# Performance work log

Hardware: AMD Instinct MI355X
Metric: run time of the kernel (lower is better)

## Reference

```python
import jax, jax.numpy as jnp
import numpy as np

N = 50000      # nodes
E = 800000     # edges (avg degree 16)
IN = 128       # in_channels = len(cfg.objects)
OC = 16        # out_channels
DIMS = [IN, 16 * OC, 8 * OC, 4 * OC, 2 * OC, OC]  # 128,256,128,64,32,16


def _glorot(key, fan_in, fan_out):
    s = jnp.sqrt(2.0 / (fan_in + fan_out)).astype(jnp.float32)
    return jax.random.normal(key, (fan_in, fan_out), jnp.float32) * s


def setup_inputs() -> dict:
    key = jax.random.key(0)
    ks = jax.random.split(key, 16)
    x = jax.random.normal(ks[0], (N, IN), jnp.float32)
    edge_index = jax.random.randint(ks[1], (2, E), 0, N, dtype=jnp.int32)
    inp = {"x": x, "edge_index": edge_index}
    # four hidden GCN layers
    names = ["1", "2", "3", "4"]
    for i, nm in enumerate(names):
        inp["W" + nm] = _glorot(ks[2 + i], DIMS[i], DIMS[i + 1])
        inp["b" + nm] = jnp.zeros((DIMS[i + 1],), jnp.float32)
    # mu / logstd heads
    inp["Wmu"] = _glorot(ks[10], DIMS[4], DIMS[5])
    inp["bmu"] = jnp.zeros((DIMS[5],), jnp.float32)
    inp["Wls"] = _glorot(ks[11], DIMS[4], DIMS[5])
    inp["bls"] = jnp.zeros((DIMS[5],), jnp.float32)
    return inp


def _gcn_norm(edge_index, n):
    # GCNConv default: add self-loops, symmetric normalization
    sl = jnp.arange(n, dtype=edge_index.dtype)
    row = jnp.concatenate([edge_index[0], sl])  # source
    col = jnp.concatenate([edge_index[1], sl])  # target
    deg = jax.ops.segment_sum(jnp.ones_like(row, jnp.float32), col, num_segments=n)
    dinv = jnp.where(deg > 0, jax.lax.rsqrt(deg), 0.0)
    norm = dinv[row] * dinv[col]  # [E + N]
    return row, col, norm


def _gcn_conv(x, W, b, row, col, norm, n):
    h = x @ W                                   # dense transform [N, F_out]
    msg = h[row] * norm[:, None]                # gather + edge scale
    return jax.ops.segment_sum(msg, col, num_segments=n) + b  # scatter-add


def reference(x, edge_index, W1, b1, W2, b2, W3, b3, W4, b4, Wmu, bmu, Wls, bls):
    n = x.shape[0]
    row, col, norm = _gcn_norm(edge_index, n)
    h = jax.nn.relu(_gcn_conv(x, W1, b1, row, col, norm, n))
    h = jax.nn.relu(_gcn_conv(h, W2, b2, row, col, norm, n))
    h = jax.nn.relu(_gcn_conv(h, W3, b3, row, col, norm, n))
    h = jax.nn.relu(_gcn_conv(h, W4, b4, row, col, norm, n))
    mu = _gcn_conv(h, Wmu, bmu, row, col, norm, n)
    logstd = _gcn_conv(h, Wls, bls, row, col, norm, n)
    return mu, logstd
```

## Files before the change

### kernel.cpp

```cpp
#include <hip/hip_runtime.h>
#include <hip/hip_bf16.h>
#include <stdint.h>

__device__ inline int imin(int a, int b) { return a < b ? a : b; }
__device__ inline int imax(int a, int b) { return a > b ? a : b; }
__device__ inline float bf2f(unsigned short u) {
    return __uint_as_float(((unsigned int)u) << 16);
}
__device__ inline unsigned short f2bf(float v) {
    unsigned int u = __float_as_uint(v);
    unsigned int r = u + 0x7FFFu + ((u >> 16) & 1u);
    return (unsigned short)(r >> 16);
}

typedef __attribute__((ext_vector_type(8))) short short8;
typedef __attribute__((ext_vector_type(4))) float floatx4;


__global__ void k_prologue(int* __restrict__ cnt, int n,
                           const float* __restrict__ x, unsigned short* __restrict__ xb, size_t nx,
                           const float* __restrict__ W1, unsigned short* __restrict__ W1T,
                           const float* __restrict__ W2, unsigned short* __restrict__ W2T,
                           const float* __restrict__ W3, unsigned short* __restrict__ W3T) {
    size_t i = (size_t)blockIdx.x * 256 + threadIdx.x;
    if (i < (size_t)n) { cnt[i] = 0; }
    size_t j = i - n;
    if (i >= (size_t)n && j < nx) { xb[j] = f2bf(x[j]); }
    size_t k = j - nx;
    const int n1 = 128 * 256, n2 = 256 * 128, n3 = 128 * 64;
    if (j >= nx && k < (size_t)(n1 + n2 + n3)) {
        int idx = (int)k;
        if (idx < n1) {
            int kk = idx >> 8, nn = idx & 255;
            W1T[nn * 128 + kk] = f2bf(W1[idx]);
        } else if (idx < n1 + n2) {
            int jj = idx - n1;
            int kk = jj >> 7, nn = jj & 127;
            W2T[nn * 256 + kk] = f2bf(W2[jj]);
        } else {
            int jj = idx - n1 - n2;
            int kk = jj >> 6, nn = jj & 63;
            W3T[nn * 128 + kk] = f2bf(W3[jj]);
        }
    }
}


__global__ void k_count(const int* __restrict__ col, int* __restrict__ cnt,
                        int* __restrict__ rank, int E, int n) {
    int e = blockIdx.x * blockDim.x + threadIdx.x;
    if (e < E) {
        int c = imax(0, imin(col[e], n - 1));
        rank[e] = atomicAdd(&cnt[c], 1);
    }
}

__global__ __launch_bounds__(256) void k_scan1(const int* __restrict__ cnt,
                                               int* __restrict__ partial,
                                               int* __restrict__ bsum, int n) {
    __shared__ int tmp[256];
    int i = blockIdx.x * 256 + threadIdx.x;
    int v = (i < n) ? ((cnt[i] + 3) & ~3) : 0;
    tmp[threadIdx.x] = v;
    __syncthreads();
    #pragma unroll
    for (int s = 1; s < 256; s <<= 1) {
        int t = (threadIdx.x >= s) ? tmp[threadIdx.x - s] : 0;
        __syncthreads();
        tmp[threadIdx.x] += t;
        __syncthreads();
    }
    if (i < n) partial[i] = tmp[threadIdx.x] - v;
    if (threadIdx.x == 255) bsum[blockIdx.x] = tmp[255];
}

__global__ __launch_bounds__(256) void k_scan2(const int* __restrict__ bsum,
                                               int* __restrict__ bsumoff, int nb) {
    __shared__ int tmp[256];
    __shared__ int carry;
    if (threadIdx.x == 0) carry = 0;
    __syncthreads();
    for (int base = 0; base < nb; base += 256) {
        int i = base + threadIdx.x;
        int v = (i < nb) ? bsum[i] : 0;
        tmp[threadIdx.x] = v;
        __syncthreads();
        #pragma unroll
        for (int s = 1; s < 256; s <<= 1) {
            int t = (threadIdx.x >= s) ? tmp[threadIdx.x - s] : 0;
            __syncthreads();
            tmp[threadIdx.x] += t;
            __syncthreads();
        }
        if (i < nb) bsumoff[i] = carry + tmp[threadIdx.x] - v;
        __syncthreads();
        if (threadIdx.x == 0) carry += tmp[255];
        __syncthreads();
    }
}

template <bool USEW>
__global__ __launch_bounds__(256) void k_scan3(const int* __restrict__ partial,
                                               const int* __restrict__ bsumoff,
                                               const int* __restrict__ cnt,
                                               int* __restrict__ offs,
                                               float* __restrict__ dinv,
                                               unsigned long long* __restrict__ edges,
                                               int* __restrict__ csr_src,
                                               int n) {
    int i = blockIdx.x * 256 + threadIdx.x;
    if (i >= n) return;
    int v = partial[i] + bsumoff[blockIdx.x];
    int c = imax(cnt[i], 0);
    offs[i] = v;
    if (i == n - 1) offs[n] = v + ((c + 3) & ~3);
    float d = (float)c + 1.0f;
    dinv[i] = rsqrtf(d);
    int end = v + ((c + 3) & ~3);
    for (int p = v + c; p < end; p++) {
        if (USEW) edges[p] = 0ull;
        else csr_src[p] = 0;
    }
}

template <bool USEW>
__global__ void k_fill(const int* __restrict__ row, const int* __restrict__ col,
                       const int* __restrict__ offs, const int* __restrict__ rank,
                       const float* __restrict__ dinv,
                       unsigned long long* __restrict__ edges, int* __restrict__ csr_src,
                       int E, int n, int cap) {
    int e = blockIdx.x * blockDim.x + threadIdx.x;
    if (e >= E) return;
    int c = imax(0, imin(col[e], n - 1));
    int r = imax(0, imin(row[e], n - 1));
    int pos = offs[c] + rank[e];
    pos = imax(0, imin(pos, cap - 1));
    if (USEW) {
        unsigned long long rec = (unsigned long long)(unsigned)r
                               | ((unsigned long long)__float_as_uint(dinv[r]) << 32);
        edges[pos] = rec;
    } else {
        csr_src[pos] = r;
    }
}


template <int NT, int FOUT, bool EPI>
__global__ __launch_bounds__(256) void k_gemm_mfma(const unsigned short* __restrict__ act,
                                                   const unsigned short* __restrict__ WT,
                                                   unsigned short* __restrict__ H,
                                                   const float* __restrict__ bias,
                                                   int nrows, int Fin) {
    constexpr int CT = NT / 16;
    __shared__ __align__(16) unsigned short sA[128 * 40];
    __shared__ __align__(16) unsigned short sB[NT * 40];
    const int tid = threadIdx.x;
    const int w = tid >> 6;
    const int lane = tid & 63;
    const int quad = lane >> 4;
    const int l15 = lane & 15;
    const int row0 = blockIdx.x * 128;
    const int col0 = blockIdx.y * NT;

    floatx4 acc[2][CT] = {};

    const int sr = tid >> 1;
    const int sp = (tid & 1) * 16;

    for (int k0 = 0; k0 < Fin; k0 += 32) {
        __syncthreads();
        {
            int grow = row0 + sr;
            uint4 v0 = make_uint4(0, 0, 0, 0), v1 = make_uint4(0, 0, 0, 0);
            if (grow < nrows) {
                const uint4* ap = (const uint4*)&act[(size_t)grow * Fin + k0 + sp];
                v0 = ap[0]; v1 = ap[1];
            }
            uint4* dst = (uint4*)&sA[sr * 40 + sp];
            dst[0] = v0; dst[1] = v1;
        }
        if (NT == 128 || tid < 128) {
            const uint4* wp = (const uint4*)&WT[(size_t)(col0 + sr) * Fin + k0 + sp];
            uint4* dst = (uint4*)&sB[sr * 40 + sp];
            dst[0] = wp[0]; dst[1] = wp[1];
        }
        __syncthreads();

        short8 bfr[CT];
        #pragma unroll
        for (int ct = 0; ct < CT; ct++)
            bfr[ct] = *(const short8*)&sB[(ct * 16 + l15) * 40 + quad * 8];
        #pragma unroll
        for (int rt = 0; rt < 2; rt++) {
            short8 afr = *(const short8*)&sA[(w * 32 + rt * 16 + l15) * 40 + quad * 8];
            #pragma unroll
            for (int ct = 0; ct < CT; ct++)
                acc[rt][ct] = __builtin_amdgcn_mfma_f32_16x16x32_bf16(afr, bfr[ct], acc[rt][ct], 0, 0, 0);
        }
    }

    #pragma unroll
    for (int rt = 0; rt < 2; rt++) {
        #pragma unroll
        for (int ct = 0; ct < CT; ct++) {
            int gcol = col0 + ct * 16 + l15;
            #pragma unroll
            for (int r = 0; r < 4; r++) {
                int grow = row0 + w * 32 + rt * 16 + quad * 4 + r;
                if (grow < nrows) {
                    float v = acc[rt][ct][r];
                    if (EPI) v = fmaxf(v + bias[gcol], 0.f);
                    H[(size_t)grow * FOUT + gcol] = f2bf(v);
                }
            }
        }
    }
}


__global__ __launch_bounds__(256) void k_gemm32(const unsigned short* __restrict__ act,
                                                const float* __restrict__ W,
                                                unsigned short* __restrict__ H,
                                                int nrows) {
    __shared__ __align__(16) float sA[32 * 68];
    __shared__ __align__(16) float sW[16 * 32];
    const int tid = threadIdx.x;
    const int row0 = blockIdx.x * 32;
    const int Fin = 64, strA = 68;

    for (int i = tid; i < 32 * Fin; i += 256) {
        int r = i >> 6;
        int k = i & 63;
        float v = 0.f;
        if (row0 + r < nrows) v = bf2f(act[(size_t)row0 * Fin + i]);
        sA[r * strA + k] = v;
    }

    const int rl = tid >> 3;
    const int cg = tid & 7;
    float a0 = 0.f, a1 = 0.f, a2 = 0.f, a3 = 0.f;

    for (int k0 = 0; k0 < Fin; k0 += 16) {
        __syncthreads();
        const float* wsrc = W + (size_t)k0 * 32;
        for (int i = tid; i < 16 * 32; i += 256) sW[i] = wsrc[i];
        __syncthreads();
        #pragma unroll 4
        for (int kk = 0; kk < 16; kk++) {
            float a = sA[rl * strA + k0 + kk];
            float4 wv = *(const float4*)&sW[kk * 32 + cg * 4];
            a0 = fmaf(a, wv.x, a0);
            a1 = fmaf(a, wv.y, a1);
            a2 = fmaf(a, wv.z, a2);
            a3 = fmaf(a, wv.w, a3);
        }
    }

    const int rowi = row0 + rl;
    if (rowi < nrows) {
        unsigned short* hp = &H[(size_t)rowi * 32 + cg * 4];
        hp[0] = f2bf(a0); hp[1] = f2bf(a1); hp[2] = f2bf(a2); hp[3] = f2bf(a3);
    }
}

__global__ void k_gemm_heads(const unsigned short* __restrict__ act,
                             const float* __restrict__ Wmu, const float* __restrict__ Wls,
                             unsigned short* __restrict__ H, int nrows) {
    int idx = blockIdx.x * blockDim.x + threadIdx.x;
    if (idx >= nrows * 32) return;
    int r = idx >> 5;
    int c = idx & 31;
    const float* Wp = (c < 16) ? Wmu : Wls;
    int cc = c & 15;
    float acc = 0.f;
    #pragma unroll 8
    for (int k = 0; k < 32; k++)
        acc = fmaf(bf2f(act[(size_t)r * 32 + k]), Wp[k * 16 + cc], acc);
    H[idx] = f2bf(acc);
}


template <int F, bool RELU, bool HASBIAS, bool USEW>
__global__ __launch_bounds__(256) void k_aggb(const unsigned short* __restrict__ Hb,
                                              unsigned short* __restrict__ out,
                                              const int* __restrict__ offs,
                                              const unsigned long long* __restrict__ edges,
                                              const int* __restrict__ src,
                                              const float* __restrict__ dinv,
                                              const float* __restrict__ bias,
                                              int nnodes, int Ecap) {
    constexpr int TPN = F / 4;
    int t = blockIdx.x * 256 + threadIdx.x;
    int node = t / TPN;
    int ln = t % TPN;
    if (node >= nnodes) return;
    int f0 = 4 * ln;

    float di = dinv[node];
    ushort4 sv = *(const ushort4*)&Hb[(size_t)node * F + f0];
    float acc0 = di * bf2f(sv.x);
    float acc1 = di * bf2f(sv.y);
    float acc2 = di * bf2f(sv.z);
    float acc3 = di * bf2f(sv.w);

    int s0 = offs[node];
    int s1 = offs[node + 1];
    s0 = imax(0, imin(s0, Ecap));
    s1 = imax(s0, imin(s1, Ecap));
    int e = s0;
    for (; e + 16 <= s1; e += 16) {
        int sr[16];
        float wv[16];
        if (USEW) {
            #pragma unroll
            for (int q = 0; q < 8; q++) {
                uint4 pr = *(const uint4*)(edges + e + 2 * q);
                sr[2 * q] = (int)pr.x;     wv[2 * q] = __uint_as_float(pr.y);
                sr[2 * q + 1] = (int)pr.z; wv[2 * q + 1] = __uint_as_float(pr.w);
            }
        } else {
            #pragma unroll
            for (int q = 0; q < 4; q++) {
                int4 a = *(const int4*)(src + e + 4 * q);
                sr[4 * q] = a.x; sr[4 * q + 1] = a.y; sr[4 * q + 2] = a.z; sr[4 * q + 3] = a.w;
            }
            #pragma unroll
            for (int q = 0; q < 16; q++) wv[q] = dinv[sr[q]];
        }
        ushort4 h[16];
        #pragma unroll
        for (int q = 0; q < 16; q++)
            h[q] = *(const ushort4*)&Hb[(size_t)sr[q] * F + f0];
        #pragma unroll
        for (int q = 0; q < 16; q++) {
            acc0 = fmaf(wv[q], bf2f(h[q].x), acc0);
            acc1 = fmaf(wv[q], bf2f(h[q].y), acc1);
            acc2 = fmaf(wv[q], bf2f(h[q].z), acc2);
            acc3 = fmaf(wv[q], bf2f(h[q].w), acc3);
        }
    }
    for (; e < s1; e += 4) {
        int sr[4];
        float wv[4];
        if (USEW) {
            uint4 p0 = *(const uint4*)(edges + e);
            uint4 p1 = *(const uint4*)(edges + e + 2);
            sr[0] = (int)p0.x; wv[0] = __uint_as_float(p0.y);
            sr[1] = (int)p0.z; wv[1] = __uint_as_float(p0.w);
            sr[2] = (int)p1.x; wv[2] = __uint_as_float(p1.y);
            sr[3] = (int)p1.z; wv[3] = __uint_as_float(p1.w);
        } else {
            int4 a = *(const int4*)(src + e);
            sr[0] = a.x; sr[1] = a.y; sr[2] = a.z; sr[3] = a.w;
            #pragma unroll
            for (int q = 0; q < 4; q++) wv[q] = dinv[sr[q]];
        }
        ushort4 h[4];
        #pragma unroll
        for (int q = 0; q < 4; q++)
            h[q] = *(const ushort4*)&Hb[(size_t)sr[q] * F + f0];
        #pragma unroll
        for (int q = 0; q < 4; q++) {
            acc0 = fmaf(wv[q], bf2f(h[q].x), acc0);
            acc1 = fmaf(wv[q], bf2f(h[q].y), acc1);
            acc2 = fmaf(wv[q], bf2f(h[q].z), acc2);
            acc3 = fmaf(wv[q], bf2f(h[q].w), acc3);
        }
    }
    float v0 = di * acc0;
    float v1 = di * acc1;
    float v2 = di * acc2;
    float v3 = di * acc3;
    if (HASBIAS) { v0 += bias[f0]; v1 += bias[f0 + 1]; v2 += bias[f0 + 2]; v3 += bias[f0 + 3]; }
    if (RELU) {
        v0 = fmaxf(v0, 0.f); v1 = fmaxf(v1, 0.f);
        v2 = fmaxf(v2, 0.f); v3 = fmaxf(v3, 0.f);
    }
    ushort4 o;
    o.x = f2bf(v0); o.y = f2bf(v1); o.z = f2bf(v2); o.w = f2bf(v3);
    *(ushort4*)&out[(size_t)node * F + f0] = o;
}

template <bool USEW>
__global__ __launch_bounds__(256) void k_agg_heads(const unsigned short* __restrict__ Hb,
                                                   float* __restrict__ out,
                                                   const int* __restrict__ offs,
                                                   const unsigned long long* __restrict__ edges,
                                                   const int* __restrict__ src,
                                                   const float* __restrict__ dinv,
                                                   const float* __restrict__ bmu, const float* __restrict__ bls,
                                                   int nnodes, int Ecap) {
    constexpr int F = 32, TPN = 8;
    int t = blockIdx.x * 256 + threadIdx.x;
    int node = t / TPN;
    int ln = t % TPN;
    if (node >= nnodes) return;
    int f0 = 4 * ln;

    float di = dinv[node];
    ushort4 sv = *(const ushort4*)&Hb[(size_t)node * F + f0];
    float acc0 = di * bf2f(sv.x);
    float acc1 = di * bf2f(sv.y);
    float acc2 = di * bf2f(sv.z);
    float acc3 = di * bf2f(sv.w);

    int s0 = offs[node];
    int s1 = offs[node + 1];
    s0 = imax(0, imin(s0, Ecap));
    s1 = imax(s0, imin(s1, Ecap));
    int e = s0;
    for (; e + 16 <= s1; e += 16) {
        int sr[16];
        float wv[16];
        if (USEW) {
            #pragma unroll
            for (int q = 0; q < 8; q++) {
                uint4 pr = *(const uint4*)(edges + e + 2 * q);
                sr[2 * q] = (int)pr.x;     wv[2 * q] = __uint_as_float(pr.y);
                sr[2 * q + 1] = (int)pr.z; wv[2 * q + 1] = __uint_as_float(pr.w);
            }
        } else {
            #pragma unroll
            for (int q = 0; q < 4; q++) {
                int4 a = *(const int4*)(src + e + 4 * q);
                sr[4 * q] = a.x; sr[4 * q + 1] = a.y; sr[4 * q + 2] = a.z; sr[4 * q + 3] = a.w;
            }
            #pragma unroll
            for (int q = 0; q < 16; q++) wv[q] = dinv[sr[q]];
        }
        ushort4 h[16];
        #pragma unroll
        for (int q = 0; q < 16; q++)
            h[q] = *(const ushort4*)&Hb[(size_t)sr[q] * F + f0];
        #pragma unroll
        for (int q = 0; q < 16; q++) {
            acc0 = fmaf(wv[q], bf2f(h[q].x), acc0);
            acc1 = fmaf(wv[q], bf2f(h[q].y), acc1);
            acc2 = fmaf(wv[q], bf2f(h[q].z), acc2);
            acc3 = fmaf(wv[q], bf2f(h[q].w), acc3);
        }
    }
    for (; e < s1; e += 4) {
        int sr[4];
        float wv[4];
        if (USEW) {
            uint4 p0 = *(const uint4*)(edges + e);
            uint4 p1 = *(const uint4*)(edges + e + 2);
            sr[0] = (int)p0.x; wv[0] = __uint_as_float(p0.y);
            sr[1] = (int)p0.z; wv[1] = __uint_as_float(p0.w);
            sr[2] = (int)p1.x; wv[2] = __uint_as_float(p1.y);
            sr[3] = (int)p1.z; wv[3] = __uint_as_float(p1.w);
        } else {
            int4 a = *(const int4*)(src + e);
            sr[0] = a.x; sr[1] = a.y; sr[2] = a.z; sr[3] = a.w;
            #pragma unroll
            for (int q = 0; q < 4; q++) wv[q] = dinv[sr[q]];
        }
        ushort4 h[4];
        #pragma unroll
        for (int q = 0; q < 4; q++)
            h[q] = *(const ushort4*)&Hb[(size_t)sr[q] * F + f0];
        #pragma unroll
        for (int q = 0; q < 4; q++) {
            acc0 = fmaf(wv[q], bf2f(h[q].x), acc0);
            acc1 = fmaf(wv[q], bf2f(h[q].y), acc1);
            acc2 = fmaf(wv[q], bf2f(h[q].z), acc2);
            acc3 = fmaf(wv[q], bf2f(h[q].w), acc3);
        }
    }
    const float* bp = (f0 < 16) ? bmu : bls;
    int fb = f0 & 15;
    float v0 = fmaf(di, acc0, bp[fb]);
    float v1 = fmaf(di, acc1, bp[fb + 1]);
    float v2 = fmaf(di, acc2, bp[fb + 2]);
    float v3 = fmaf(di, acc3, bp[fb + 3]);
    float* op = (f0 < 16) ? (out + (size_t)node * 16 + fb)
                          : (out + (size_t)nnodes * 16 + (size_t)node * 16 + fb);
    *(float4*)op = make_float4(v0, v1, v2, v3);
}


template <bool USEW>
static void run_pipeline(void* const* d_in, void* d_out, void* d_ws,
                         int N, int E, hipStream_t stream) {
    const float* x  = (const float*)d_in[0];
    const int* ei   = (const int*)d_in[1];
    const float* W1 = (const float*)d_in[2];
    const float* b1 = (const float*)d_in[3];
    const float* W2 = (const float*)d_in[4];
    const float* b2 = (const float*)d_in[5];
    const float* W3 = (const float*)d_in[6];
    const float* b3 = (const float*)d_in[7];
    const float* W4 = (const float*)d_in[8];
    const float* b4 = (const float*)d_in[9];
    const float* Wmu = (const float*)d_in[10];
    const float* bmu = (const float*)d_in[11];
    const float* Wls = (const float*)d_in[12];
    const float* bls = (const float*)d_in[13];
    const int* row = ei;
    const int* col = ei + E;
    const int nb = (N + 255) / 256;
    const int E8 = E + 8 * N;

    auto align16 = [](char* p) {
        return (char*)(((uintptr_t)p + 15) & ~(uintptr_t)15);
    };
    char* p = (char*)d_ws;
    unsigned short* act = (unsigned short*)p;    p += (size_t)N * 256 * 2;
    unsigned short* H = (unsigned short*)p;      p += (size_t)N * 256 * 2;
    unsigned short* xb = H;
    unsigned short* xa = (unsigned short*)p;     p += (size_t)N * 128 * 2;
    float* dinv = (float*)p;                     p += (size_t)N * 4;
    int* cnt = (int*)p;                          p += (size_t)N * 4;
    int* offs = (int*)p;                         p += (size_t)(N + 1) * 4;
    int* partial = (int*)p;                      p += (size_t)N * 4;
    int* bsum = (int*)p;                         p += (size_t)nb * 4;
    int* bsumoff = (int*)p;                      p += (size_t)nb * 4;
    p = align16(p);
    int* rank = (int*)p;                         p += (size_t)E * 4;
    p = align16(p);
    unsigned short* W1T = (unsigned short*)p;    p += 256 * 128 * 2;
    unsigned short* W2T = (unsigned short*)p;    p += 128 * 256 * 2;
    unsigned short* W3T = (unsigned short*)p;    p += 64 * 128 * 2;
    p = align16(p);
    unsigned long long* edges = nullptr;
    int* csr_src = nullptr;
    if (USEW) edges = (unsigned long long*)p;
    else      csr_src = (int*)p;

    {
        size_t total = (size_t)N + (size_t)N * 128 + (128 * 256 + 256 * 128 + 128 * 64);
        k_prologue<<<(unsigned)((total + 255) / 256), 256, 0, stream>>>(
            cnt, N, x, xb, (size_t)N * 128, W1, W1T, W2, W2T, W3, W3T);
    }
    k_count<<<(E + 255) / 256, 256, 0, stream>>>(col, cnt, rank, E, N);
    k_scan1<<<nb, 256, 0, stream>>>(cnt, partial, bsum, N);
    k_scan2<<<1, 256, 0, stream>>>(bsum, bsumoff, nb);
    k_scan3<USEW><<<nb, 256, 0, stream>>>(partial, bsumoff, cnt, offs, dinv, edges, csr_src, N);
    k_fill<USEW><<<(E + 255) / 256, 256, 0, stream>>>(row, col, offs, rank, dinv, edges, csr_src, E, N, E8);

    const int gx = (N + 127) / 128;
    k_aggb<128, false, false, USEW><<<(unsigned)(((size_t)N * 32 + 255) / 256), 256, 0, stream>>>(xb, xa, offs, edges, csr_src, dinv, nullptr, N, E8);
    k_gemm_mfma<128, 256, true><<<dim3(gx, 2), 256, 0, stream>>>(xa, W1T, act, b1, N, 128);
    k_gemm_mfma<128, 128, false><<<dim3(gx, 1), 256, 0, stream>>>(act, W2T, H, nullptr, N, 256);
    k_aggb<128, true, true, USEW><<<(unsigned)(((size_t)N * 32 + 255) / 256), 256, 0, stream>>>(H, act, offs, edges, csr_src, dinv, b2, N, E8);
    k_gemm_mfma<64, 64, false><<<dim3(gx, 1), 256, 0, stream>>>(act, W3T, H, nullptr, N, 128);
    k_aggb<64, true, true, USEW><<<(unsigned)(((size_t)N * 16 + 255) / 256), 256, 0, stream>>>(H, act, offs, edges, csr_src, dinv, b3, N, E8);
    k_gemm32<<<(N + 31) / 32, 256, 0, stream>>>(act, W4, H, N);
    k_aggb<32, true, true, USEW><<<(unsigned)(((size_t)N * 8 + 255) / 256), 256, 0, stream>>>(H, act, offs, edges, csr_src, dinv, b4, N, E8);
    float* outF = (float*)d_out;
    k_gemm_heads<<<(unsigned)(((size_t)N * 32 + 255) / 256), 256, 0, stream>>>(act, Wmu, Wls, H, N);
    k_agg_heads<USEW><<<(unsigned)(((size_t)N * 8 + 255) / 256), 256, 0, stream>>>(H, outF, offs, edges, csr_src, dinv, bmu, bls, N, E8);
}

extern "C" void kernel_launch(void* const* d_in, const int* in_sizes, int n_in,
                              void* d_out, int out_size, void* d_ws, size_t ws_size,
                              hipStream_t stream) {
    const int N = in_sizes[0] / 128;
    const int E = in_sizes[1] / 2;
    const int nb = (N + 255) / 256;
    const size_t E8 = (size_t)E + 8 * (size_t)N;

    size_t fixed = (size_t)N * 256 * 2 * 2 + (size_t)N * 128 * 2
                 + (size_t)N * 4 * 4 + 4 + (size_t)nb * 8 + (size_t)E * 4
                 + (256 * 128 + 128 * 256 + 64 * 128) * 2 + 128;
    size_t need_w = fixed + E8 * 8;
    if (ws_size >= need_w)
        run_pipeline<true>(d_in, d_out, d_ws, N, E, stream);
    else
        run_pipeline<false>(d_in, d_out, d_ws, N, E, stream);
}
```

Baseline: 351.0 us.

## Fuse whole GCN pipeline into one cooperative persistent kernel with grid syncs

Replaces about fifteen separate kernel launches (CSR build, scans, aggregations, GEMMs, heads) with a single cooperative kernel of 512 blocks. The phases run as grid-stride loops separated by grid.sync(). The aim is to remove per-launch overhead and the idle gaps between dependent kernels. In exchange, occupancy is capped at 512 blocks with launch_bounds(256,2), each phase pays a grid-wide barrier, and the GEMM and aggregation work is tiled less flexibly. The old multi-kernel path is kept as a fallback if the cooperative launch fails.

```diff
diff --git a/kernel.cpp b/kernel.cpp
--- a/kernel.cpp
+++ b/kernel.cpp
@@ -1,6 +1,9 @@
 #include <hip/hip_runtime.h>
+#include <hip/hip_cooperative_groups.h>
 #include <hip/hip_bf16.h>
 #include <stdint.h>
+
+namespace cg = cooperative_groups;
 
 __device__ inline int imin(int a, int b) { return a < b ? a : b; }
 __device__ inline int imax(int a, int b) { return a > b ? a : b; }
@@ -17,18 +20,17 @@
 typedef __attribute__((ext_vector_type(4))) float floatx4;
 
 
-__global__ void k_prologue(int* __restrict__ cnt, int n,
-                           const float* __restrict__ x, unsigned short* __restrict__ xb, size_t nx,
-                           const float* __restrict__ W1, unsigned short* __restrict__ W1T,
-                           const float* __restrict__ W2, unsigned short* __restrict__ W2T,
-                           const float* __restrict__ W3, unsigned short* __restrict__ W3T) {
-    size_t i = (size_t)blockIdx.x * 256 + threadIdx.x;
-    if (i < (size_t)n) { cnt[i] = 0; }
+__device__ inline void prologue_elem(size_t i, int n, int* __restrict__ cnt,
+                                     const float* __restrict__ x, unsigned short* __restrict__ xb, size_t nx,
+                                     const float* __restrict__ W1, unsigned short* __restrict__ W1T,
+                                     const float* __restrict__ W2, unsigned short* __restrict__ W2T,
+                                     const float* __restrict__ W3, unsigned short* __restrict__ W3T) {
+    if (i < (size_t)n) { cnt[i] = 0; return; }
     size_t j = i - n;
-    if (i >= (size_t)n && j < nx) { xb[j] = f2bf(x[j]); }
+    if (j < nx) { xb[j] = f2bf(x[j]); return; }
     size_t k = j - nx;
     const int n1 = 128 * 256, n2 = 256 * 128, n3 = 128 * 64;
-    if (j >= nx && k < (size_t)(n1 + n2 + n3)) {
+    if (k < (size_t)(n1 + n2 + n3)) {
         int idx = (int)k;
         if (idx < n1) {
             int kk = idx >> 8, nn = idx & 255;
@@ -45,72 +47,54 @@
     }
 }
 
-
-__global__ void k_count(const int* __restrict__ col, int* __restrict__ cnt,
-                        int* __restrict__ rank, int E, int n) {
-    int e = blockIdx.x * blockDim.x + threadIdx.x;
-    if (e < E) {
-        int c = imax(0, imin(col[e], n - 1));
-        rank[e] = atomicAdd(&cnt[c], 1);
-    }
-}
-
-__global__ __launch_bounds__(256) void k_scan1(const int* __restrict__ cnt,
-                                               int* __restrict__ partial,
-                                               int* __restrict__ bsum, int n) {
-    __shared__ int tmp[256];
-    int i = blockIdx.x * 256 + threadIdx.x;
+__device__ inline void scan1_chunk(int chunk, int tid, int* __restrict__ tmp,
+                                   const int* __restrict__ cnt,
+                                   int* __restrict__ partial, int* __restrict__ bsum, int n) {
+    int i = chunk * 256 + tid;
     int v = (i < n) ? ((cnt[i] + 3) & ~3) : 0;
-    tmp[threadIdx.x] = v;
+    tmp[tid] = v;
     __syncthreads();
     #pragma unroll
     for (int s = 1; s < 256; s <<= 1) {
-        int t = (threadIdx.x >= s) ? tmp[threadIdx.x - s] : 0;
+        int t = (tid >= s) ? tmp[tid - s] : 0;
         __syncthreads();
-        tmp[threadIdx.x] += t;
+        tmp[tid] += t;
         __syncthreads();
     }
-    if (i < n) partial[i] = tmp[threadIdx.x] - v;
-    if (threadIdx.x == 255) bsum[blockIdx.x] = tmp[255];
-}
-
-__global__ __launch_bounds__(256) void k_scan2(const int* __restrict__ bsum,
-                                               int* __restrict__ bsumoff, int nb) {
-    __shared__ int tmp[256];
-    __shared__ int carry;
-    if (threadIdx.x == 0) carry = 0;
+    if (i < n) partial[i] = tmp[tid] - v;
+    if (tid == 255) bsum[chunk] = tmp[255];
+}
+
+__device__ inline void scan2_block(int tid, int* __restrict__ tmp, int* __restrict__ carry,
+                                   const int* __restrict__ bsum, int* __restrict__ bsumoff, int nb) {
+    if (tid == 0) *carry = 0;
     __syncthreads();
     for (int base = 0; base < nb; base += 256) {
-        int i = base + threadIdx.x;
+        int i = base + tid;
         int v = (i < nb) ? bsum[i] : 0;
-        tmp[threadIdx.x] = v;
+        tmp[tid] = v;
         __syncthreads();
         #pragma unroll
         for (int s = 1; s < 256; s <<= 1) {
-            int t = (threadIdx.x >= s) ? tmp[threadIdx.x - s] : 0;
+            int t = (tid >= s) ? tmp[tid - s] : 0;
             __syncthreads();
-            tmp[threadIdx.x] += t;
+            tmp[tid] += t;
             __syncthreads();
         }
-        if (i < nb) bsumoff[i] = carry + tmp[threadIdx.x] - v;
+        if (i < nb) bsumoff[i] = *carry + tmp[tid] - v;
         __syncthreads();
-        if (threadIdx.x == 0) carry += tmp[255];
+        if (tid == 0) *carry += tmp[255];
         __syncthreads();
     }
 }
 
 template <bool USEW>
-__global__ __launch_bounds__(256) void k_scan3(const int* __restrict__ partial,
-                                               const int* __restrict__ bsumoff,
-                                               const int* __restrict__ cnt,
-                                               int* __restrict__ offs,
-                                               float* __restrict__ dinv,
-                                               unsigned long long* __restrict__ edges,
-                                               int* __restrict__ csr_src,
-                                               int n) {
-    int i = blockIdx.x * 256 + threadIdx.x;
-    if (i >= n) return;
-    int v = partial[i] + bsumoff[blockIdx.x];
+__device__ inline void scan3_elem(int i, int boff,
+                                  const int* __restrict__ partial, const int* __restrict__ cnt,
+                                  int* __restrict__ offs, float* __restrict__ dinv,
+                                  unsigned long long* __restrict__ edges, int* __restrict__ csr_src,
+                                  int n) {
+    int v = partial[i] + boff;
     int c = imax(cnt[i], 0);
     offs[i] = v;
     if (i == n - 1) offs[n] = v + ((c + 3) & ~3);
@@ -124,13 +108,11 @@
 }
 
 template <bool USEW>
-__global__ void k_fill(const int* __restrict__ row, const int* __restrict__ col,
-                       const int* __restrict__ offs, const int* __restrict__ rank,
-                       const float* __restrict__ dinv,
-                       unsigned long long* __restrict__ edges, int* __restrict__ csr_src,
-                       int E, int n, int cap) {
-    int e = blockIdx.x * blockDim.x + threadIdx.x;
-    if (e >= E) return;
+__device__ inline void fill_elem(int e, const int* __restrict__ row, const int* __restrict__ col,
+                                 const int* __restrict__ offs, const int* __restrict__ rank,
+                                 const float* __restrict__ dinv,
+                                 unsigned long long* __restrict__ edges, int* __restrict__ csr_src,
+                                 int n, int cap) {
     int c = imax(0, imin(col[e], n - 1));
     int r = imax(0, imin(row[e], n - 1));
     int pos = offs[c] + rank[e];
@@ -146,21 +128,19 @@
 
 
 template <int NT, int FOUT, bool EPI>
-__global__ __launch_bounds__(256) void k_gemm_mfma(const unsigned short* __restrict__ act,
-                                                   const unsigned short* __restrict__ WT,
-                                                   unsigned short* __restrict__ H,
-                                                   const float* __restrict__ bias,
-                                                   int nrows, int Fin) {
+__device__ void gemm_tile(const unsigned short* __restrict__ act,
+                          const unsigned short* __restrict__ WT,
+                          unsigned short* __restrict__ H,
+                          const float* __restrict__ bias,
+                          int nrows, int Fin, int bx, int by, int tid,
+                          unsigned short* __restrict__ sA, unsigned short* __restrict__ sB) {
     constexpr int CT = NT / 16;
-    __shared__ __align__(16) unsigned short sA[128 * 40];
-    __shared__ __align__(16) unsigned short sB[NT * 40];
-    const int tid = threadIdx.x;
     const int w = tid >> 6;
     const int lane = tid & 63;
     const int quad = lane >> 4;
     const int l15 = lane & 15;
-    const int row0 = blockIdx.x * 128;
-    const int col0 = blockIdx.y * NT;
+    const int row0 = bx * 128;
+    const int col0 = by * NT;
 
     floatx4 acc[2][CT] = {};
 
@@ -218,15 +198,15 @@
 }
 
 
-__global__ __launch_bounds__(256) void k_gemm32(const unsigned short* __restrict__ act,
-                                                const float* __restrict__ W,
-                                                unsigned short* __restrict__ H,
-                                                int nrows) {
-    __shared__ __align__(16) float sA[32 * 68];
-    __shared__ __align__(16) float sW[16 * 32];
-    const int tid = threadIdx.x;
-    const int row0 = blockIdx.x * 32;
+__device__ void gemm32_tile(const unsigned short* __restrict__ act,
+                            const float* __restrict__ W,
+                            unsigned short* __restrict__ H,
+                            int nrows, int bx, int tid,
+                            float* __restrict__ sA, float* __restrict__ sW) {
+    const int row0 = bx * 32;
     const int Fin = 64, strA = 68;
+
+    __syncthreads();
 
     for (int i = tid; i < 32 * Fin; i += 256) {
         int r = i >> 6;
@@ -234,10 +214,11 @@
         float v = 0.f;
         if (row0 + r < nrows) v = bf2f(act[(size_t)row0 * Fin + i]);
         sA[r * strA + k] = v;
+        (void)k;
     }
 
     const int rl = tid >> 3;
-    const int cg = tid & 7;
+    const int cg_ = tid & 7;
     float a0 = 0.f, a1 = 0.f, a2 = 0.f, a3 = 0.f;
 
     for (int k0 = 0; k0 < Fin; k0 += 16) {
@@ -248,7 +229,7 @@
         #pragma unroll 4
         for (int kk = 0; kk < 16; kk++) {
             float a = sA[rl * strA + k0 + kk];
-            float4 wv = *(const float4*)&sW[kk * 32 + cg * 4];
+            float4 wv = *(const float4*)&sW[kk * 32 + cg_ * 4];
             a0 = fmaf(a, wv.x, a0);
             a1 = fmaf(a, wv.y, a1);
             a2 = fmaf(a, wv.z, a2);
@@ -258,16 +239,14 @@
 
     const int rowi = row0 + rl;
     if (rowi < nrows) {
-        unsigned short* hp = &H[(size_t)rowi * 32 + cg * 4];
+        unsigned short* hp = &H[(size_t)rowi * 32 + cg_ * 4];
         hp[0] = f2bf(a0); hp[1] = f2bf(a1); hp[2] = f2bf(a2); hp[3] = f2bf(a3);
     }
 }
 
-__global__ void k_gemm_heads(const unsigned short* __restrict__ act,
-                             const float* __restrict__ Wmu, const float* __restrict__ Wls,
-                             unsigned short* __restrict__ H, int nrows) {
-    int idx = blockIdx.x * blockDim.x + threadIdx.x;
-    if (idx >= nrows * 32) return;
+__device__ inline void heads_one(int idx, const unsigned short* __restrict__ act,
+                                 const float* __restrict__ Wmu, const float* __restrict__ Wls,
+                                 unsigned short* __restrict__ H) {
     int r = idx >> 5;
     int c = idx & 31;
     const float* Wp = (c < 16) ? Wmu : Wls;
@@ -281,19 +260,15 @@
 
 
 template <int F, bool RELU, bool HASBIAS, bool USEW>
-__global__ __launch_bounds__(256) void k_aggb(const unsigned short* __restrict__ Hb,
-                                              unsigned short* __restrict__ out,
-                                              const int* __restrict__ offs,
-                                              const unsigned long long* __restrict__ edges,
-                                              const int* __restrict__ src,
-                                              const float* __restrict__ dinv,
-                                              const float* __restrict__ bias,
-                                              int nnodes, int Ecap) {
-    constexpr int TPN = F / 4;
-    int t = blockIdx.x * 256 + threadIdx.x;
-    int node = t / TPN;
-    int ln = t % TPN;
-    if (node >= nnodes) return;
+__device__ inline void agg_one(int node, int ln,
+                               const unsigned short* __restrict__ Hb,
+                               unsigned short* __restrict__ out,
+                               const int* __restrict__ offs,
+                               const unsigned long long* __restrict__ edges,
+                               const int* __restrict__ src,
+                               const float* __restrict__ dinv,
+                               const float* __restrict__ bias,
+                               int Ecap) {
     int f0 = 4 * ln;
 
     float di = dinv[node];
@@ -382,19 +357,16 @@
 }
 
 template <bool USEW>
-__global__ __launch_bounds__(256) void k_agg_heads(const unsigned short* __restrict__ Hb,
-                                                   float* __restrict__ out,
-                                                   const int* __restrict__ offs,
-                                                   const unsigned long long* __restrict__ edges,
-                                                   const int* __restrict__ src,
-                                                   const float* __restrict__ dinv,
-                                                   const float* __restrict__ bmu, const float* __restrict__ bls,
-                                                   int nnodes, int Ecap) {
-    constexpr int F = 32, TPN = 8;
-    int t = blockIdx.x * 256 + threadIdx.x;
-    int node = t / TPN;
-    int ln = t % TPN;
-    if (node >= nnodes) return;
+__device__ inline void agg_heads_one(int node, int ln,
+                                     const unsigned short* __restrict__ Hb,
+                                     float* __restrict__ out,
+                                     const int* __restrict__ offs,
+                                     const unsigned long long* __restrict__ edges,
+                                     const int* __restrict__ src,
+                                     const float* __restrict__ dinv,
+                                     const float* __restrict__ bmu, const float* __restrict__ bls,
+                                     int nnodes, int Ecap) {
+    constexpr int F = 32;
     int f0 = 4 * ln;
 
     float di = dinv[node];
@@ -479,6 +451,267 @@
     *(float4*)op = make_float4(v0, v1, v2, v3);
 }
 
+
+struct MegaP {
+    const float* x;
+    const int* row; const int* col;
+    const float *W1, *b1, *W2, *b2, *W3, *b3, *W4, *b4, *Wmu, *bmu, *Wls, *bls;
+    unsigned short *act, *H, *xb, *xa, *W1T, *W2T, *W3T;
+    float* dinv;
+    int *cnt, *offs, *partial, *bsum, *bsumoff, *rank;
+    unsigned long long* edges;
+    int* csr_src;
+    float* outF;
+    int N, E, nb, E8;
+};
+
+template <int F, bool RELU, bool HASBIAS, bool USEW>
+__device__ inline void agg_phase(long long g0, long long T,
+                                 const unsigned short* Hb, unsigned short* out,
+                                 const float* bias, const MegaP& P) {
+    constexpr int TPN = F / 4;
+    long long total = (long long)P.N * TPN;
+    for (long long t = g0; t < total; t += T) {
+        int node = (int)(t / TPN);
+        int ln = (int)(t % TPN);
+        agg_one<F, RELU, HASBIAS, USEW>(node, ln, Hb, out, P.offs, P.edges, P.csr_src,
+                                        P.dinv, bias, P.E8);
+    }
+}
+
+template <bool USEW>
+__global__ __launch_bounds__(256, 2) void k_mega(MegaP P) {
+    cg::grid_group grid = cg::this_grid();
+    __shared__ __align__(16) unsigned char SMEM[20480];
+    const int tid = threadIdx.x;
+    const int G = gridDim.x;
+    const long long T = (long long)G * 256;
+    const long long g0 = (long long)blockIdx.x * 256 + tid;
+
+    {
+        size_t total = (size_t)P.N + (size_t)P.N * 128 + (128 * 256 + 256 * 128 + 128 * 64);
+        for (size_t i = (size_t)g0; i < total; i += (size_t)T)
+            prologue_elem(i, P.N, P.cnt, P.x, P.xb, (size_t)P.N * 128,
+                          P.W1, P.W1T, P.W2, P.W2T, P.W3, P.W3T);
+    }
+    grid.sync();
+    for (long long e = g0; e < P.E; e += T) {
+        int c = imax(0, imin(P.col[e], P.N - 1));
+        P.rank[e] = atomicAdd(&P.cnt[c], 1);
+    }
+    grid.sync();
+    {
+        int* tmp = (int*)SMEM;
+        for (int chunk = blockIdx.x; chunk < P.nb; chunk += G) {
+            __syncthreads();
+            scan1_chunk(chunk, tid, tmp, P.cnt, P.partial, P.bsum, P.N);
+        }
+    }
+    grid.sync();
+    if (blockIdx.x == 0) {
+        int* tmp = (int*)SMEM;
+        int* carry = (int*)(SMEM + 1024);
+        scan2_block(tid, tmp, carry, P.bsum, P.bsumoff, P.nb);
+    }
+    grid.sync();
+    for (long long i = g0; i < P.N; i += T)
+        scan3_elem<USEW>((int)i, P.bsumoff[i >> 8], P.partial, P.cnt,
+                         P.offs, P.dinv, P.edges, P.csr_src, P.N);
+    grid.sync();
+    for (long long e = g0; e < P.E; e += T)
+        fill_elem<USEW>((int)e, P.row, P.col, P.offs, P.rank, P.dinv,
+                        P.edges, P.csr_src, P.N, P.E8);
+    grid.sync();
+    agg_phase<128, false, false, USEW>(g0, T, P.xb, P.xa, nullptr, P);
+    grid.sync();
+    {
+        unsigned short* sA = (unsigned short*)SMEM;
+        unsigned short* sB = sA + 128 * 40;
+        int gx = (P.N + 127) >> 7;
+        for (int tile = blockIdx.x; tile < gx * 2; tile += G)
+            gemm_tile<128, 256, true>(P.xa, P.W1T, P.act, P.b1, P.N, 128,
+                                      tile % gx, tile / gx, tid, sA, sB);
+    }
+    grid.sync();
+    {
+        unsigned short* sA = (unsigned short*)SMEM;
+        unsigned short* sB = sA + 128 * 40;
+        int gx = (P.N + 127) >> 7;
+        for (int tile = blockIdx.x; tile < gx; tile += G)
+            gemm_tile<128, 128, false>(P.act, P.W2T, P.H, nullptr, P.N, 256,
+                                       tile, 0, tid, sA, sB);
+    }
+    grid.sync();
+    agg_phase<128, true, true, USEW>(g0, T, P.H, P.act, P.b2, P);
+    grid.sync();
+    {
+        unsigned short* sA = (unsigned short*)SMEM;
+        unsigned short* sB = sA + 128 * 40;
+        int gx = (P.N + 127) >> 7;
+        for (int tile = blockIdx.x; tile < gx; tile += G)
+            gemm_tile<64, 64, false>(P.act, P.W3T, P.H, nullptr, P.N, 128,
+                                     tile, 0, tid, sA, sB);
+    }
+    grid.sync();
+    agg_phase<64, true, true, USEW>(g0, T, P.H, P.act, P.b3, P);
+    grid.sync();
+    {
+        float* sA32 = (float*)SMEM;
+        float* sW = (float*)(SMEM + 32 * 68 * 4);
+        int nt = (P.N + 31) >> 5;
+        for (int tile = blockIdx.x; tile < nt; tile += G)
+            gemm32_tile(P.act, P.W4, P.H, P.N, tile, tid, sA32, sW);
+    }
+    grid.sync();
+    agg_phase<32, true, true, USEW>(g0, T, P.H, P.act, P.b4, P);
+    grid.sync();
+    for (long long idx = g0; idx < (long long)P.N * 32; idx += T)
+        heads_one((int)idx, P.act, P.Wmu, P.Wls, P.H);
+    grid.sync();
+    {
+        constexpr int TPN = 8;
+        long long total = (long long)P.N * TPN;
+        for (long long t = g0; t < total; t += T) {
+            int node = (int)(t / TPN);
+            int ln = (int)(t % TPN);
+            agg_heads_one<USEW>(node, ln, P.H, P.outF, P.offs, P.edges, P.csr_src,
+                                P.dinv, P.bmu, P.bls, P.N, P.E8);
+        }
+    }
+}
+
+
+__global__ void k_prologue(int* cnt, int n, const float* x, unsigned short* xb, size_t nx,
+                           const float* W1, unsigned short* W1T,
+                           const float* W2, unsigned short* W2T,
+                           const float* W3, unsigned short* W3T) {
+    size_t i = (size_t)blockIdx.x * 256 + threadIdx.x;
+    size_t total = (size_t)n + nx + (128 * 256 + 256 * 128 + 128 * 64);
+    if (i < total) prologue_elem(i, n, cnt, x, xb, nx, W1, W1T, W2, W2T, W3, W3T);
+}
+
+__global__ void k_count(const int* col, int* cnt, int* rank, int E, int n) {
+    int e = blockIdx.x * blockDim.x + threadIdx.x;
+    if (e < E) {
+        int c = imax(0, imin(col[e], n - 1));
+        rank[e] = atomicAdd(&cnt[c], 1);
+    }
+}
+
+__global__ __launch_bounds__(256) void k_scan1(const int* cnt, int* partial, int* bsum, int n) {
+    __shared__ int tmp[256];
+    scan1_chunk(blockIdx.x, threadIdx.x, tmp, cnt, partial, bsum, n);
+}
+
+__global__ __launch_bounds__(256) void k_scan2(const int* bsum, int* bsumoff, int nb) {
+    __shared__ int tmp[256];
+    __shared__ int carry;
+    scan2_block(threadIdx.x, tmp, &carry, bsum, bsumoff, nb);
+}
+
+template <bool USEW>
+__global__ __launch_bounds__(256) void k_scan3(const int* partial, const int* bsumoff,
+                                               const int* cnt, int* offs, float* dinv,
+                                               unsigned long long* edges, int* csr_src, int n) {
+    int i = blockIdx.x * 256 + threadIdx.x;
+    if (i < n)
+        scan3_elem<USEW>(i, bsumoff[blockIdx.x], partial, cnt, offs, dinv, edges, csr_src, n);
+}
+
+template <bool USEW>
+__global__ void k_fill(const int* row, const int* col, const int* offs, const int* rank,
+                       const float* dinv, unsigned long long* edges, int* csr_src,
+                       int E, int n, int cap) {
+    int e = blockIdx.x * blockDim.x + threadIdx.x;
+    if (e < E) fill_elem<USEW>(e, row, col, offs, rank, dinv, edges, csr_src, n, cap);
+}
+
+template <int NT, int FOUT, bool EPI>
+__global__ __launch_bounds__(256) void k_gemm_mfma(const unsigned short* act,
+                                                   const unsigned short* WT,
+                                                   unsigned short* H, const float* bias,
+                                                   int nrows, int Fin) {
+    __shared__ __align__(16) unsigned short sA[128 * 40];
+    __shared__ __align__(16) unsigned short sB[NT * 40];
+    gemm_tile<NT, FOUT, EPI>(act, WT, H, bias, nrows, Fin, blockIdx.x, blockIdx.y,
+                             threadIdx.x, sA, sB);
+}
+
+__global__ __launch_bounds__(256) void k_gemm32(const unsigned short* act, const float* W,
+                                                unsigned short* H, int nrows) {
+    __shared__ __align__(16) float sA[32 * 68];
+    __shared__ __align__(16) float sW[16 * 32];
+    gemm32_tile(act, W, H, nrows, blockIdx.x, threadIdx.x, sA, sW);
+}
+
+__global__ void k_gemm_heads(const unsigned short* act, const float* Wmu, const float* Wls,
+                             unsigned short* H, int nrows) {
+    int idx = blockIdx.x * blockDim.x + threadIdx.x;
+    if (idx < nrows * 32) heads_one(idx, act, Wmu, Wls, H);
+}
+
+template <int F, bool RELU, bool HASBIAS, bool USEW>
+__global__ __launch_bounds__(256) void k_aggb(const unsigned short* Hb, unsigned short* out,
+                                              const int* offs, const unsigned long long* edges,
+                                              const int* src, const float* dinv,
+                                              const float* bias, int nnodes, int Ecap) {
+    constexpr int TPN = F / 4;
+    int t = blockIdx.x * 256 + threadIdx.x;
+    int node = t / TPN;
+    int ln = t % TPN;
+    if (node < nnodes)
+        agg_one<F, RELU, HASBIAS, USEW>(node, ln, Hb, out, offs, edges, src, dinv, bias, Ecap);
+}
+
+template <bool USEW>
+__global__ __launch_bounds__(256) void k_agg_heads(const unsigned short* Hb, float* out,
+                                                   const int* offs, const unsigned long long* edges,
+                                                   const int* src, const float* dinv,
+                                                   const float* bmu, const float* bls,
+                                                   int nnodes, int Ecap) {
+    constexpr int TPN = 8;
+    int t = blockIdx.x * 256 + threadIdx.x;
+    int node = t / TPN;
+    int ln = t % TPN;
+    if (node < nnodes)
+        agg_heads_one<USEW>(node, ln, Hb, out, offs, edges, src, dinv, bmu, bls, nnodes, Ecap);
+}
+
+
+struct WsLayout {
+    unsigned short *act, *H, *xb, *xa, *W1T, *W2T, *W3T;
+    float* dinv;
+    int *cnt, *offs, *partial, *bsum, *bsumoff, *rank;
+    unsigned long long* edges;
+    int* csr_src;
+};
+
+static WsLayout layout_ws(void* d_ws, int N, int E, bool usew) {
+    auto align16 = [](char* p) { return (char*)(((uintptr_t)p + 15) & ~(uintptr_t)15); };
+    const int nb = (N + 255) / 256;
+    WsLayout L;
+    char* p = (char*)d_ws;
+    L.act = (unsigned short*)p;   p += (size_t)N * 256 * 2;
+    L.H = (unsigned short*)p;     p += (size_t)N * 256 * 2;
+    L.xb = L.H;
+    L.xa = (unsigned short*)p;    p += (size_t)N * 128 * 2;
+    L.dinv = (float*)p;           p += (size_t)N * 4;
+    L.cnt = (int*)p;              p += (size_t)N * 4;
+    L.offs = (int*)p;             p += (size_t)(N + 1) * 4;
+    L.partial = (int*)p;          p += (size_t)N * 4;
+    L.bsum = (int*)p;             p += (size_t)nb * 4;
+    L.bsumoff = (int*)p;          p += (size_t)nb * 4;
+    p = align16(p);
+    L.rank = (int*)p;             p += (size_t)E * 4;
+    p = align16(p);
+    L.W1T = (unsigned short*)p;   p += 256 * 128 * 2;
+    L.W2T = (unsigned short*)p;   p += 128 * 256 * 2;
+    L.W3T = (unsigned short*)p;   p += 64 * 128 * 2;
+    p = align16(p);
+    L.edges = usew ? (unsigned long long*)p : nullptr;
+    L.csr_src = usew ? nullptr : (int*)p;
+    return L;
+}
 
 template <bool USEW>
 static void run_pipeline(void* const* d_in, void* d_out, void* d_ws,
@@ -502,55 +735,31 @@
     const int nb = (N + 255) / 256;
     const int E8 = E + 8 * N;
 
-    auto align16 = [](char* p) {
-        return (char*)(((uintptr_t)p + 15) & ~(uintptr_t)15);
-    };
-    char* p = (char*)d_ws;
-    unsigned short* act = (unsigned short*)p;    p += (size_t)N * 256 * 2;
-    unsigned short* H = (unsigned short*)p;      p += (size_t)N * 256 * 2;
-    unsigned short* xb = H;
-    unsigned short* xa = (unsigned short*)p;     p += (size_t)N * 128 * 2;
-    float* dinv = (float*)p;                     p += (size_t)N * 4;
-    int* cnt = (int*)p;                          p += (size_t)N * 4;
-    int* offs = (int*)p;                         p += (size_t)(N + 1) * 4;
-    int* partial = (int*)p;                      p += (size_t)N * 4;
-    int* bsum = (int*)p;                         p += (size_t)nb * 4;
-    int* bsumoff = (int*)p;                      p += (size_t)nb * 4;
-    p = align16(p);
-    int* rank = (int*)p;                         p += (size_t)E * 4;
-    p = align16(p);
-    unsigned short* W1T = (unsigned short*)p;    p += 256 * 128 * 2;
-    unsigned short* W2T = (unsigned short*)p;    p += 128 * 256 * 2;
-    unsigned short* W3T = (unsigned short*)p;    p += 64 * 128 * 2;
-    p = align16(p);
-    unsigned long long* edges = nullptr;
-    int* csr_src = nullptr;
-    if (USEW) edges = (unsigned long long*)p;
-    else      csr_src = (int*)p;
+    WsLayout L = layout_ws(d_ws, N, E, USEW);
 
     {
         size_t total = (size_t)N + (size_t)N * 128 + (128 * 256 + 256 * 128 + 128 * 64);
         k_prologue<<<(unsigned)((total + 255) / 256), 256, 0, stream>>>(
-            cnt, N, x, xb, (size_t)N * 128, W1, W1T, W2, W2T, W3, W3T);
-    }
-    k_count<<<(E + 255) / 256, 256, 0, stream>>>(col, cnt, rank, E, N);
-    k_scan1<<<nb, 256, 0, stream>>>(cnt, partial, bsum, N);
-    k_scan2<<<1, 256, 0, stream>>>(bsum, bsumoff, nb);
-    k_scan3<USEW><<<nb, 256, 0, stream>>>(partial, bsumoff, cnt, offs, dinv, edges, csr_src, N);
-    k_fill<USEW><<<(E + 255) / 256, 256, 0, stream>>>(row, col, offs, rank, dinv, edges, csr_src, E, N, E8);
+            L.cnt, N, x, L.xb, (size_t)N * 128, W1, L.W1T, W2, L.W2T, W3, L.W3T);
+    }
+    k_count<<<(E + 255) / 256, 256, 0, stream>>>(col, L.cnt, L.rank, E, N);
+    k_scan1<<<nb, 256, 0, stream>>>(L.cnt, L.partial, L.bsum, N);
+    k_scan2<<<1, 256, 0, stream>>>(L.bsum, L.bsumoff, nb);
+    k_scan3<USEW><<<nb, 256, 0, stream>>>(L.partial, L.bsumoff, L.cnt, L.offs, L.dinv, L.edges, L.csr_src, N);
+    k_fill<USEW><<<(E + 255) / 256, 256, 0, stream>>>(row, col, L.offs, L.rank, L.dinv, L.edges, L.csr_src, E, N, E8);
 
     const int gx = (N + 127) / 128;
-    k_aggb<128, false, false, USEW><<<(unsigned)(((size_t)N * 32 + 255) / 256), 256, 0, stream>>>(xb, xa, offs, edges, csr_src, dinv, nullptr, N, E8);
-    k_gemm_mfma<128, 256, true><<<dim3(gx, 2), 256, 0, stream>>>(xa, W1T, act, b1, N, 128);
-    k_gemm_mfma<128, 128, false><<<dim3(gx, 1), 256, 0, stream>>>(act, W2T, H, nullptr, N, 256);
-    k_aggb<128, true, true, USEW><<<(unsigned)(((size_t)N * 32 + 255) / 256), 256, 0, stream>>>(H, act, offs, edges, csr_src, dinv, b2, N, E8);
-    k_gemm_mfma<64, 64, false><<<dim3(gx, 1), 256, 0, stream>>>(act, W3T, H, nullptr, N, 128);
-    k_aggb<64, true, true, USEW><<<(unsigned)(((size_t)N * 16 + 255) / 256), 256, 0, stream>>>(H, act, offs, edges, csr_src, dinv, b3, N, E8);
-    k_gemm32<<<(N + 31) / 32, 256, 0, stream>>>(act, W4, H, N);
-    k_aggb<32, true, true, USEW><<<(unsigned)(((size_t)N * 8 + 255) / 256), 256, 0, stream>>>(H, act, offs, edges, csr_src, dinv, b4, N, E8);
+    k_aggb<128, false, false, USEW><<<(unsigned)(((size_t)N * 32 + 255) / 256), 256, 0, stream>>>(L.xb, L.xa, L.offs, L.edges, L.csr_src, L.dinv, nullptr, N, E8);
+    k_gemm_mfma<128, 256, true><<<dim3(gx, 2), 256, 0, stream>>>(L.xa, L.W1T, L.act, b1, N, 128);
+    k_gemm_mfma<128, 128, false><<<dim3(gx, 1), 256, 0, stream>>>(L.act, L.W2T, L.H, nullptr, N, 256);
+    k_aggb<128, true, true, USEW><<<(unsigned)(((size_t)N * 32 + 255) / 256), 256, 0, stream>>>(L.H, L.act, L.offs, L.edges, L.csr_src, L.dinv, b2, N, E8);
+    k_gemm_mfma<64, 64, false><<<dim3(gx, 1), 256, 0, stream>>>(L.act, L.W3T, L.H, nullptr, N, 128);
+    k_aggb<64, true, true, USEW><<<(unsigned)(((size_t)N * 16 + 255) / 256), 256, 0, stream>>>(L.H, L.act, L.offs, L.edges, L.csr_src, L.dinv, b3, N, E8);
+    k_gemm32<<<(N + 31) / 32, 256, 0, stream>>>(L.act, W4, L.H, N);
+    k_aggb<32, true, true, USEW><<<(unsigned)(((size_t)N * 8 + 255) / 256), 256, 0, stream>>>(L.H, L.act, L.offs, L.edges, L.csr_src, L.dinv, b4, N, E8);
     float* outF = (float*)d_out;
-    k_gemm_heads<<<(unsigned)(((size_t)N * 32 + 255) / 256), 256, 0, stream>>>(act, Wmu, Wls, H, N);
-    k_agg_heads<USEW><<<(unsigned)(((size_t)N * 8 + 255) / 256), 256, 0, stream>>>(H, outF, offs, edges, csr_src, dinv, bmu, bls, N, E8);
+    k_gemm_heads<<<(unsigned)(((size_t)N * 32 + 255) / 256), 256, 0, stream>>>(L.act, Wmu, Wls, L.H, N);
+    k_agg_heads<USEW><<<(unsigned)(((size_t)N * 8 + 255) / 256), 256, 0, stream>>>(L.H, outF, L.offs, L.edges, L.csr_src, L.dinv, bmu, bls, N, E8);
 }
 
 extern "C" void kernel_launch(void* const* d_in, const int* in_sizes, int n_in,
@@ -559,14 +768,44 @@
     const int N = in_sizes[0] / 128;
     const int E = in_sizes[1] / 2;
     const int nb = (N + 255) / 256;
-    const size_t E8 = (size_t)E + 8 * (size_t)N;
+    const size_t E8cap = (size_t)E + 8 * (size_t)N;
 
     size_t fixed = (size_t)N * 256 * 2 * 2 + (size_t)N * 128 * 2
                  + (size_t)N * 4 * 4 + 4 + (size_t)nb * 8 + (size_t)E * 4
                  + (256 * 128 + 128 * 256 + 64 * 128) * 2 + 128;
-    size_t need_w = fixed + E8 * 8;
-    if (ws_size >= need_w)
-        run_pipeline<true>(d_in, d_out, d_ws, N, E, stream);
+    size_t need_w = fixed + E8cap * 8;
+    bool usew = (ws_size >= need_w);
+
+    WsLayout L = layout_ws(d_ws, N, E, usew);
+
+    MegaP P;
+    P.x = (const float*)d_in[0];
+    P.row = (const int*)d_in[1];
+    P.col = (const int*)d_in[1] + E;
+    P.W1 = (const float*)d_in[2];  P.b1 = (const float*)d_in[3];
+    P.W2 = (const float*)d_in[4];  P.b2 = (const float*)d_in[5];
+    P.W3 = (const float*)d_in[6];  P.b3 = (const float*)d_in[7];
+    P.W4 = (const float*)d_in[8];  P.b4 = (const float*)d_in[9];
+    P.Wmu = (const float*)d_in[10]; P.bmu = (const float*)d_in[11];
+    P.Wls = (const float*)d_in[12]; P.bls = (const float*)d_in[13];
+    P.act = L.act; P.H = L.H; P.xb = L.xb; P.xa = L.xa;
+    P.W1T = L.W1T; P.W2T = L.W2T; P.W3T = L.W3T;
+    P.dinv = L.dinv; P.cnt = L.cnt; P.offs = L.offs; P.partial = L.partial;
+    P.bsum = L.bsum; P.bsumoff = L.bsumoff; P.rank = L.rank;
+    P.edges = L.edges; P.csr_src = L.csr_src;
+    P.outF = (float*)d_out;
+    P.N = N; P.E = E; P.nb = nb; P.E8 = E + 8 * N;
+
+    void* kargs[] = { (void*)&P };
+    hipError_t err;
+    if (usew)
+        err = hipLaunchCooperativeKernel((const void*)k_mega<true>, dim3(512), dim3(256),
+                                         kargs, 0, stream);
     else
-        run_pipeline<false>(d_in, d_out, d_ws, N, E, stream);
-}
+        err = hipLaunchCooperativeKernel((const void*)k_mega<false>, dim3(512), dim3(256),
+                                         kargs, 0, stream);
+    if (err != hipSuccess) {
+        if (usew) run_pipeline<true>(d_in, d_out, d_ws, N, E, stream);
+        else      run_pipeline<false>(d_in, d_out, d_ws, N, E, stream);
+    }
+}
```

Result: slower. 1.304 ms (+271.5%).
